# Kernel optimization log

Measured on AMD Instinct MI355X. Metric: run time of the kernel, lower is better.

The kernel has to match this reference:

```python
import jax, jax.numpy as jnp
import numpy as np

N_NODES = 100_000
N_EDGES = 800_000
D = 96
BN_EPS = 1e-5
LEAKY_SLOPE = 0.01


def setup_inputs() -> dict:
    key = jax.random.key(0)
    ks = jax.random.split(key, 9)
    x = jax.random.normal(ks[0], (N_NODES, D), dtype=jnp.float32)
    edge_index = jax.random.randint(ks[1], (2, N_EDGES), 0, N_NODES, dtype=jnp.int64)
    s = 0.05
    return {
        "x": x,
        "edge_index": edge_index,
        # SAGEConv #1 (mean aggregator, bias=False)
        "W_self1": jax.random.normal(ks[2], (D, D), dtype=jnp.float32) * s,
        "W_neigh1": jax.random.normal(ks[3], (D, D), dtype=jnp.float32) * s,
        # SAGEConv #2 (pool aggregator): fc_pool has bias, fc_self/fc_neigh bias=False
        "W_pool": jax.random.normal(ks[4], (D, D), dtype=jnp.float32) * s,
        "b_pool": jax.random.normal(ks[5], (D,), dtype=jnp.float32) * s,
        "W_self2": jax.random.normal(ks[6], (D, D), dtype=jnp.float32) * s,
        "W_neigh2": jax.random.normal(ks[7], (D, D), dtype=jnp.float32) * s,
        # BatchNorm affine params
        "g1": jnp.ones((D,), jnp.float32),
        "beta1": jnp.zeros((D,), jnp.float32),
        "g2": jnp.ones((D,), jnp.float32),
        "beta2": jnp.zeros((D,), jnp.float32),
    }


def _batch_norm(h, gamma, beta):
    # training-mode BatchNorm1d: biased batch stats over nodes
    mu = h.mean(axis=0)
    var = jnp.mean(jnp.square(h - mu), axis=0)
    return gamma * (h - mu) * jax.lax.rsqrt(var + BN_EPS) + beta


def _forward(x, edge_index, W_self1, W_neigh1, W_pool, b_pool, W_self2, W_neigh2,
             g1, beta1, g2, beta2):
    src, dst = edge_index[0], edge_index[1]
    n = x.shape[0]
    deg = jax.ops.segment_sum(jnp.ones((src.shape[0],), x.dtype), dst, num_segments=n)

    # ---- SAGEConv (mean): h_neigh = mean_{u in N(v)} x_u ; out = x W_self + h_neigh W_neigh
    agg_sum = jax.ops.segment_sum(x[src], dst, num_segments=n)          # [N, D]
    h_mean = agg_sum / jnp.maximum(deg, 1.0)[:, None]                   # 0 for isolated nodes
    out1 = x @ W_self1 + h_mean @ W_neigh1
    out1 = _batch_norm(out1, g1, beta1)

    # ---- SAGEConv (pool): h_neigh = max_{u in N(v)} relu(x_u W_pool + b_pool)
    hp = jax.nn.relu(x @ W_pool + b_pool)                               # [N, D]
    agg_max = jax.ops.segment_max(hp[src], dst, num_segments=n)        # -inf where empty
    h_max = jnp.where(deg[:, None] > 0, agg_max, 0.0)
    out2 = x @ W_self2 + h_max @ W_neigh2
    out2 = _batch_norm(out2, g2, beta2)

    return jax.nn.leaky_relu(out1 + out2, negative_slope=LEAKY_SLOPE)


def reference(x, edge_index, W_self1, W_neigh1, W_pool, b_pool, W_self2, W_neigh2,
              g1, beta1, g2, beta2):
    return _forward(x, edge_index, W_self1, W_neigh1, W_pool, b_pool,
                    W_self2, W_neigh2, g1, beta1, g2, beta2)
```

## Files before the change

kernel.cpp:

```cpp
#include <hip/hip_runtime.h>

#define NN 100000
#define NE 800000
#define DD 96
#define NROWPAD 100096
#define GBLK 782
#define SCAN_BLOCKS 100
#define SCAN_CHUNK 1000

typedef __attribute__((ext_vector_type(8))) short bf16x8;
typedef __attribute__((ext_vector_type(8))) unsigned short u16x8;
typedef __attribute__((ext_vector_type(4))) float f32x4;
typedef unsigned short u16;
typedef unsigned int u32;

#define MFMA16 __builtin_amdgcn_mfma_f32_16x16x32_bf16

#define OFF_DEG      0u
#define OFF_ROWSTART 100000u
#define OFF_CURSOR   200004u
#define OFF_BSUM     300004u
#define OFF_STATS    302180u
#define OFF_WT       302948u
#define OFF_CSR      325988u
#define OFF_XH       1125988u
#define OFF_HMBF     10735204u
#define OFF_HXBF     15539812u

__device__ __forceinline__ u16 f2b(float f) {
  u32 u = __float_as_uint(f);
  u += 0x7FFFu + ((u >> 16) & 1u);
  return (u16)(u >> 16);
}
__device__ __forceinline__ float b2f(short h) {
  return __uint_as_float(((u32)(u16)h) << 16);
}

__global__ void wprep_kernel(const float* __restrict__ Ws1, const float* __restrict__ Wn1,
                             const float* __restrict__ Ws2, const float* __restrict__ Wn2,
                             const float* __restrict__ Wp, u16* __restrict__ wt) {
  int idx = blockIdx.x * 256 + threadIdx.x;
  if (idx >= 5 * 9216) return;
  int m = idx / 9216, r = idx % 9216;
  int k = r / 96, c = r % 96;
  const float* W = (m == 0) ? Ws1 : (m == 1) ? Wn1 : (m == 2) ? Ws2 : (m == 3) ? Wn2 : Wp;
  wt[m * 9216 + c * 96 + k] = f2b(W[k * 96 + c]);
}

__global__ void deg_kernel(const int* __restrict__ dst, int* __restrict__ deg) {
  int e = blockIdx.x * blockDim.x + threadIdx.x;
  if (e >= NE) return;
  atomicAdd(&deg[dst[e]], 1);
}

__global__ void scan_sum_kernel(const int* __restrict__ deg, int* __restrict__ bsum) {
  __shared__ int red[256];
  int t = threadIdx.x;
  int base = blockIdx.x * SCAN_CHUNK;
  int s = 0;
  for (int i = t; i < SCAN_CHUNK; i += 256) s += deg[base + i];
  red[t] = s;
  __syncthreads();
  for (int off = 128; off > 0; off >>= 1) {
    if (t < off) red[t] += red[t + off];
    __syncthreads();
  }
  if (t == 0) bsum[blockIdx.x] = red[0];
}

__global__ void scan_bsum_kernel(int* __restrict__ bsum, int* __restrict__ row_start) {
  __shared__ int sm[128];
  int t = threadIdx.x;
  int v = (t < SCAN_BLOCKS) ? bsum[t] : 0;
  sm[t] = v;
  __syncthreads();
  for (int off = 1; off < 128; off <<= 1) {
    int u = 0;
    if (t >= off) u = sm[t - off];
    __syncthreads();
    if (t >= off) sm[t] += u;
    __syncthreads();
  }
  if (t < SCAN_BLOCKS) bsum[t] = sm[t] - v;
  if (t == SCAN_BLOCKS - 1) row_start[NN] = sm[t];
}

__global__ void scan_final_kernel(const int* __restrict__ deg,
                                  const int* __restrict__ bsum,
                                  int* __restrict__ row_start,
                                  int* __restrict__ cursor) {
  __shared__ int sm[256];
  int t = threadIdx.x;
  int base = blockIdx.x * SCAN_CHUNK + t * 4;
  int4 d = {0, 0, 0, 0};
  if (t < 250) d = *reinterpret_cast<const int4*>(deg + base);
  int tot = d.x + d.y + d.z + d.w;
  sm[t] = tot;
  __syncthreads();
  for (int off = 1; off < 256; off <<= 1) {
    int u = 0;
    if (t >= off) u = sm[t - off];
    __syncthreads();
    if (t >= off) sm[t] += u;
    __syncthreads();
  }
  if (t < 250) {
    int run = bsum[blockIdx.x] + sm[t] - tot;
    int4 rs;
    rs.x = run;
    rs.y = run + d.x;
    rs.z = run + d.x + d.y;
    rs.w = run + d.x + d.y + d.z;
    *reinterpret_cast<int4*>(row_start + base) = rs;
    *reinterpret_cast<int4*>(cursor + base) = rs;
  }
}

__global__ void fill_csr_kernel(const int* __restrict__ src,
                                const int* __restrict__ dst,
                                int* __restrict__ cursor,
                                int* __restrict__ csr) {
  int e = blockIdx.x * blockDim.x + threadIdx.x;
  if (e >= NE) return;
  int pos = atomicAdd(&cursor[dst[e]], 1);
  csr[pos] = src[e];
}

__global__ __launch_bounds__(512) void hp_gemm_kernel(const float* __restrict__ x,
                                                      const u16* __restrict__ wt,
                                                      const float* __restrict__ bp,
                                                      u16* __restrict__ xh) {
  __shared__ bf16x8 wl[1152];
  int t = threadIdx.x;
  const bf16x8* wg = reinterpret_cast<const bf16x8*>(wt + 4 * 9216);
  for (int j = t; j < 1152; j += 512) wl[j] = wg[j];
  __syncthreads();
  int w = t >> 6, lane = t & 63;
  int i = lane & 15, g = lane >> 4;
  int row_base = blockIdx.x * 128 + w * 16;
  int grow_a = row_base + i;
  int lrow = grow_a < NN ? grow_a : NN - 1;
  const float4* xr = reinterpret_cast<const float4*>(x + (size_t)lrow * 96);
  bf16x8* xhv = reinterpret_cast<bf16x8*>(xh);
  bf16x8 ax[3];
#pragma unroll
  for (int kb = 0; kb < 3; ++kb) {
    float4 p = xr[(kb * 4 + g) * 2];
    float4 q = xr[(kb * 4 + g) * 2 + 1];
    bf16x8 v;
    v[0] = (short)f2b(p.x); v[1] = (short)f2b(p.y); v[2] = (short)f2b(p.z); v[3] = (short)f2b(p.w);
    v[4] = (short)f2b(q.x); v[5] = (short)f2b(q.y); v[6] = (short)f2b(q.z); v[7] = (short)f2b(q.w);
    ax[kb] = v;
    xhv[(size_t)grow_a * 24 + kb * 4 + g] = v;
  }
  for (int nt = 0; nt < 6; ++nt) {
    f32x4 acc = {0.f, 0.f, 0.f, 0.f};
    int bch = (nt * 16 + i) * 12;
#pragma unroll
    for (int kb = 0; kb < 3; ++kb)
      acc = MFMA16(ax[kb], wl[bch + kb * 4 + g], acc, 0, 0, 0);
    int col = nt * 16 + i;
    float bias = bp[col];
#pragma unroll
    for (int r = 0; r < 4; ++r) {
      int grow = row_base + g * 4 + r;
      xh[(size_t)grow * 192 + 96 + col] = f2b(fmaxf(acc[r] + bias, 0.0f));
    }
  }
}

__global__ __launch_bounds__(256) void gather_kernel(const u16* __restrict__ xh,
                                                     const int* __restrict__ row_start,
                                                     const int* __restrict__ csr,
                                                     u16* __restrict__ hmbf,
                                                     u16* __restrict__ hxbf) {
  int t = threadIdx.x;
  int node = blockIdx.x * 32 + (t & 31);
  int slot = t >> 5;
  bool isMax = slot >= 4;
  if (node >= NN) return;
  int beg = row_start[node], end = row_start[node + 1];
  int last = (end > beg) ? (end - 1) : 0;
  int cbase = slot * 3;
  const u16x8* XH = reinterpret_cast<const u16x8*>(xh);
  float s0[8], s1[8], s2[8];
  u16x8 m0, m1, m2;
#pragma unroll
  for (int j = 0; j < 8; ++j) {
    s0[j] = 0.f; s1[j] = 0.f; s2[j] = 0.f;
    m0[j] = 0; m1[j] = 0; m2[j] = 0;
  }
  int e = beg;
  int i0 = csr[(beg < end) ? beg : 0];
  int i1 = csr[(beg + 1 <= last) ? beg + 1 : last];
  int i2 = csr[(beg + 2 <= last) ? beg + 2 : last];
  int i3 = csr[(beg + 3 <= last) ? beg + 3 : last];
  for (; e + 4 <= end; e += 4) {
    int p = e + 4;
    int n0 = csr[(p     <= last) ? p     : last];
    int n1 = csr[(p + 1 <= last) ? p + 1 : last];
    int n2 = csr[(p + 2 <= last) ? p + 2 : last];
    int n3 = csr[(p + 3 <= last) ? p + 3 : last];
    size_t b0 = (size_t)i0 * 24 + cbase;
    size_t b1 = (size_t)i1 * 24 + cbase;
    size_t b2 = (size_t)i2 * 24 + cbase;
    size_t b3 = (size_t)i3 * 24 + cbase;
    u16x8 a0 = XH[b0], a1 = XH[b0 + 1], a2 = XH[b0 + 2];
    u16x8 c0 = XH[b1], c1 = XH[b1 + 1], c2 = XH[b1 + 2];
    u16x8 d0 = XH[b2], d1 = XH[b2 + 1], d2 = XH[b2 + 2];
    u16x8 f0 = XH[b3], f1 = XH[b3 + 1], f2 = XH[b3 + 2];
    if (isMax) {
#pragma unroll
      for (int j = 0; j < 8; ++j) {
        u16 p0 = a0[j] > c0[j] ? a0[j] : c0[j];
        u16 q0 = d0[j] > f0[j] ? d0[j] : f0[j];
        u16 r0 = p0 > q0 ? p0 : q0;
        m0[j] = m0[j] > r0 ? m0[j] : r0;
        u16 p1 = a1[j] > c1[j] ? a1[j] : c1[j];
        u16 q1 = d1[j] > f1[j] ? d1[j] : f1[j];
        u16 r1 = p1 > q1 ? p1 : q1;
        m1[j] = m1[j] > r1 ? m1[j] : r1;
        u16 p2 = a2[j] > c2[j] ? a2[j] : c2[j];
        u16 q2 = d2[j] > f2[j] ? d2[j] : f2[j];
        u16 r2 = p2 > q2 ? p2 : q2;
        m2[j] = m2[j] > r2 ? m2[j] : r2;
      }
    } else {
#pragma unroll
      for (int j = 0; j < 8; ++j) {
        s0[j] += (b2f((short)a0[j]) + b2f((short)c0[j])) + (b2f((short)d0[j]) + b2f((short)f0[j]));
        s1[j] += (b2f((short)a1[j]) + b2f((short)c1[j])) + (b2f((short)d1[j]) + b2f((short)f1[j]));
        s2[j] += (b2f((short)a2[j]) + b2f((short)c2[j])) + (b2f((short)d2[j]) + b2f((short)f2[j]));
      }
    }
    i0 = n0; i1 = n1; i2 = n2; i3 = n3;
  }
  int rem = end - e;
#pragma unroll
  for (int k = 0; k < 3; ++k) {
    if (k < rem) {
      int ik = (k == 0) ? i0 : (k == 1) ? i1 : i2;
      size_t b0 = (size_t)ik * 24 + cbase;
      u16x8 a0 = XH[b0], a1 = XH[b0 + 1], a2 = XH[b0 + 2];
      if (isMax) {
#pragma unroll
        for (int j = 0; j < 8; ++j) {
          m0[j] = m0[j] > a0[j] ? m0[j] : a0[j];
          m1[j] = m1[j] > a1[j] ? m1[j] : a1[j];
          m2[j] = m2[j] > a2[j] ? m2[j] : a2[j];
        }
      } else {
#pragma unroll
        for (int j = 0; j < 8; ++j) {
          s0[j] += b2f((short)a0[j]);
          s1[j] += b2f((short)a1[j]);
          s2[j] += b2f((short)a2[j]);
        }
      }
    }
  }
  if (isMax) {
    u16x8* dv = reinterpret_cast<u16x8*>(hxbf);
    size_t ob = (size_t)node * 12 + (slot - 4) * 3;
    dv[ob] = m0; dv[ob + 1] = m1; dv[ob + 2] = m2;
  } else {
    float scl = (end > beg) ? 1.0f / (float)(end - beg) : 0.0f;
    u16x8 w0, w1, w2;
#pragma unroll
    for (int j = 0; j < 8; ++j) {
      w0[j] = f2b(s0[j] * scl);
      w1[j] = f2b(s1[j] * scl);
      w2[j] = f2b(s2[j] * scl);
    }
    u16x8* dv = reinterpret_cast<u16x8*>(hmbf);
    size_t ob = (size_t)node * 12 + slot * 3;
    dv[ob] = w0; dv[ob + 1] = w1; dv[ob + 2] = w2;
  }
}

__global__ __launch_bounds__(512, 6) void stats_gemm_kernel(const u16* __restrict__ xh,
                                                            const u16* __restrict__ hmbf,
                                                            const u16* __restrict__ hxbf,
                                                            const u16* __restrict__ wt,
                                                            float* __restrict__ stats) {
  __shared__ bf16x8 wl[2304];
  __shared__ float smst[384];
  int t = threadIdx.x;
  const bf16x8* wg = reinterpret_cast<const bf16x8*>(wt);
  for (int j = t; j < 2304; j += 512) wl[j] = wg[j];
  for (int j = t; j < 384; j += 512) smst[j] = 0.f;
  __syncthreads();
  int w = t >> 6, lane = t & 63;
  int i = lane & 15, g = lane >> 4;
  int row_base = blockIdx.x * 128 + w * 16;
  size_t arowx = (size_t)(row_base + i) * 24;
  size_t arowh = (size_t)(row_base + i) * 12;
  const bf16x8* X = reinterpret_cast<const bf16x8*>(xh);
  const bf16x8* M = reinterpret_cast<const bf16x8*>(hmbf);
  const bf16x8* H = reinterpret_cast<const bf16x8*>(hxbf);
  bf16x8 ax0 = X[arowx + g], ax1 = X[arowx + 4 + g], ax2 = X[arowx + 8 + g];
  {
    bf16x8 am0 = M[arowh + g], am1 = M[arowh + 4 + g], am2 = M[arowh + 8 + g];
#pragma unroll
    for (int nt = 0; nt < 6; ++nt) {
      f32x4 a1 = {0.f, 0.f, 0.f, 0.f};
      int bch = (nt * 16 + i) * 12 + g;
      a1 = MFMA16(ax0, wl[bch], a1, 0, 0, 0);
      a1 = MFMA16(ax1, wl[bch + 4], a1, 0, 0, 0);
      a1 = MFMA16(ax2, wl[bch + 8], a1, 0, 0, 0);
      a1 = MFMA16(am0, wl[1152 + bch], a1, 0, 0, 0);
      a1 = MFMA16(am1, wl[1152 + bch + 4], a1, 0, 0, 0);
      a1 = MFMA16(am2, wl[1152 + bch + 8], a1, 0, 0, 0);
      int col = nt * 16 + i;
      float s1 = 0, q1 = 0;
#pragma unroll
      for (int r = 0; r < 4; ++r) {
        int grow = row_base + g * 4 + r;
        if (grow < NN) { float v = a1[r]; s1 += v; q1 += v * v; }
      }
      s1 += __shfl_xor(s1, 16); q1 += __shfl_xor(q1, 16);
      s1 += __shfl_xor(s1, 32); q1 += __shfl_xor(q1, 32);
      if (g == 0) {
        atomicAdd(&smst[col], s1);
        atomicAdd(&smst[96 + col], q1);
      }
    }
  }
  __syncthreads();
  for (int j = t; j < 2304; j += 512) wl[j] = wg[2304 + j];
  __syncthreads();
  {
    bf16x8 ah0 = H[arowh + g], ah1 = H[arowh + 4 + g], ah2 = H[arowh + 8 + g];
#pragma unroll
    for (int nt = 0; nt < 6; ++nt) {
      f32x4 a2 = {0.f, 0.f, 0.f, 0.f};
      int bch = (nt * 16 + i) * 12 + g;
      a2 = MFMA16(ax0, wl[bch], a2, 0, 0, 0);
      a2 = MFMA16(ax1, wl[bch + 4], a2, 0, 0, 0);
      a2 = MFMA16(ax2, wl[bch + 8], a2, 0, 0, 0);
      a2 = MFMA16(ah0, wl[1152 + bch], a2, 0, 0, 0);
      a2 = MFMA16(ah1, wl[1152 + bch + 4], a2, 0, 0, 0);
      a2 = MFMA16(ah2, wl[1152 + bch + 8], a2, 0, 0, 0);
      int col = nt * 16 + i;
      float s2 = 0, q2 = 0;
#pragma unroll
      for (int r = 0; r < 4; ++r) {
        int grow = row_base + g * 4 + r;
        if (grow < NN) { float v = a2[r]; s2 += v; q2 += v * v; }
      }
      s2 += __shfl_xor(s2, 16); q2 += __shfl_xor(q2, 16);
      s2 += __shfl_xor(s2, 32); q2 += __shfl_xor(q2, 32);
      if (g == 0) {
        atomicAdd(&smst[192 + col], s2);
        atomicAdd(&smst[288 + col], q2);
      }
    }
  }
  __syncthreads();
  for (int j = t; j < 384; j += 512) atomicAdd(&stats[j], smst[j]);
}

__global__ __launch_bounds__(512, 4) void out_gemm_kernel(const u16* __restrict__ xh,
                                                          const u16* __restrict__ hmbf,
                                                          const u16* __restrict__ hxbf,
                                                          const u16* __restrict__ wt,
                                                          const float* __restrict__ stats,
                                                          const float* __restrict__ g1,
                                                          const float* __restrict__ beta1,
                                                          const float* __restrict__ g2,
                                                          const float* __restrict__ beta2,
                                                          float* __restrict__ out) {
  __shared__ bf16x8 wl[2304];
  __shared__ float pl[384];
  int t = threadIdx.x;
  const bf16x8* wg = reinterpret_cast<const bf16x8*>(wt);
  for (int j = t; j < 2304; j += 512) wl[j] = wg[j];
  if (t < 96) {
    const float inv_n = 1.0f / NN;
    float mu1 = stats[t] * inv_n;
    float var1 = fmaxf(stats[96 + t] * inv_n - mu1 * mu1, 0.0f);
    float a1 = g1[t] * rsqrtf(var1 + 1e-5f);
    pl[t] = a1;
    pl[96 + t] = beta1[t] - a1 * mu1;
    float mu2 = stats[192 + t] * inv_n;
    float var2 = fmaxf(stats[288 + t] * inv_n - mu2 * mu2, 0.0f);
    float a2 = g2[t] * rsqrtf(var2 + 1e-5f);
    pl[192 + t] = a2;
    pl[288 + t] = beta2[t] - a2 * mu2;
  }
  __syncthreads();
  int w = t >> 6, lane = t & 63;
  int i = lane & 15, g = lane >> 4;
  int row_base = blockIdx.x * 128 + w * 16;
  size_t arowx = (size_t)(row_base + i) * 24;
  size_t arowh = (size_t)(row_base + i) * 12;
  const bf16x8* X = reinterpret_cast<const bf16x8*>(xh);
  const bf16x8* M = reinterpret_cast<const bf16x8*>(hmbf);
  const bf16x8* H = reinterpret_cast<const bf16x8*>(hxbf);
  bf16x8 ax0 = X[arowx + g], ax1 = X[arowx + 4 + g], ax2 = X[arowx + 8 + g];
  f32x4 o1[6];
  {
    bf16x8 am0 = M[arowh + g], am1 = M[arowh + 4 + g], am2 = M[arowh + 8 + g];
#pragma unroll
    for (int nt = 0; nt < 6; ++nt) {
      f32x4 a1 = {0.f, 0.f, 0.f, 0.f};
      int bch = (nt * 16 + i) * 12 + g;
      a1 = MFMA16(ax0, wl[bch], a1, 0, 0, 0);
      a1 = MFMA16(ax1, wl[bch + 4], a1, 0, 0, 0);
      a1 = MFMA16(ax2, wl[bch + 8], a1, 0, 0, 0);
      a1 = MFMA16(am0, wl[1152 + bch], a1, 0, 0, 0);
      a1 = MFMA16(am1, wl[1152 + bch + 4], a1, 0, 0, 0);
      a1 = MFMA16(am2, wl[1152 + bch + 8], a1, 0, 0, 0);
      o1[nt] = a1;
    }
  }
  __syncthreads();
  for (int j = t; j < 2304; j += 512) wl[j] = wg[2304 + j];
  __syncthreads();
  {
    bf16x8 ah0 = H[arowh + g], ah1 = H[arowh + 4 + g], ah2 = H[arowh + 8 + g];
#pragma unroll
    for (int nt = 0; nt < 6; ++nt) {
      f32x4 a2 = {0.f, 0.f, 0.f, 0.f};
      int bch = (nt * 16 + i) * 12 + g;
      a2 = MFMA16(ax0, wl[bch], a2, 0, 0, 0);
      a2 = MFMA16(ax1, wl[bch + 4], a2, 0, 0, 0);
      a2 = MFMA16(ax2, wl[bch + 8], a2, 0, 0, 0);
      a2 = MFMA16(ah0, wl[1152 + bch], a2, 0, 0, 0);
      a2 = MFMA16(ah1, wl[1152 + bch + 4], a2, 0, 0, 0);
      a2 = MFMA16(ah2, wl[1152 + bch + 8], a2, 0, 0, 0);
      int col = nt * 16 + i;
      float p1 = pl[col], c1 = pl[96 + col];
      float p2 = pl[192 + col], c2 = pl[288 + col];
#pragma unroll
      for (int r = 0; r < 4; ++r) {
        int grow = row_base + g * 4 + r;
        if (grow < NN) {
          float v = p1 * o1[nt][r] + c1 + p2 * a2[r] + c2;
          v = v > 0.f ? v : 0.01f * v;
          out[(size_t)grow * 96 + col] = v;
        }
      }
    }
  }
}

extern "C" void kernel_launch(void* const* d_in, const int* in_sizes, int n_in,
                              void* d_out, int out_size, void* d_ws, size_t ws_size,
                              hipStream_t stream) {
  const float* x       = (const float*)d_in[0];
  const int*   ei      = (const int*)d_in[1];
  const float* W_self1 = (const float*)d_in[2];
  const float* W_neigh1= (const float*)d_in[3];
  const float* W_pool  = (const float*)d_in[4];
  const float* b_pool  = (const float*)d_in[5];
  const float* W_self2 = (const float*)d_in[6];
  const float* W_neigh2= (const float*)d_in[7];
  const float* g1      = (const float*)d_in[8];
  const float* beta1   = (const float*)d_in[9];
  const float* g2      = (const float*)d_in[10];
  const float* beta2   = (const float*)d_in[11];
  float* out = (float*)d_out;

  float* ws = (float*)d_ws;
  int*   deg       = (int*)(ws + OFF_DEG);
  int*   row_start = (int*)(ws + OFF_ROWSTART);
  int*   cursor    = (int*)(ws + OFF_CURSOR);
  int*   bsum      = (int*)(ws + OFF_BSUM);
  float* stats     = ws + OFF_STATS;
  u16*   wt        = (u16*)(ws + OFF_WT);
  int*   csr       = (int*)(ws + OFF_CSR);
  u16*   xh        = (u16*)(ws + OFF_XH);
  u16*   hmbf      = (u16*)(ws + OFF_HMBF);
  u16*   hxbf      = (u16*)(ws + OFF_HXBF);

  const int* src = ei;
  const int* dst = ei + NE;

  hipMemsetAsync(deg, 0, NN * sizeof(int), stream);
  hipMemsetAsync(stats, 0, 384 * sizeof(float), stream);

  wprep_kernel<<<(5 * 9216 + 255) / 256, 256, 0, stream>>>(W_self1, W_neigh1, W_self2,
                                                           W_neigh2, W_pool, wt);

  deg_kernel<<<(NE + 255) / 256, 256, 0, stream>>>(dst, deg);
  scan_sum_kernel<<<SCAN_BLOCKS, 256, 0, stream>>>(deg, bsum);
  scan_bsum_kernel<<<1, 128, 0, stream>>>(bsum, row_start);
  scan_final_kernel<<<SCAN_BLOCKS, 256, 0, stream>>>(deg, bsum, row_start, cursor);
  fill_csr_kernel<<<(NE + 255) / 256, 256, 0, stream>>>(src, dst, cursor, csr);

  hp_gemm_kernel<<<GBLK, 512, 0, stream>>>(x, wt, b_pool, xh);

  gather_kernel<<<(NN + 31) / 32, 256, 0, stream>>>(xh, row_start, csr, hmbf, hxbf);

  stats_gemm_kernel<<<GBLK, 512, 0, stream>>>(xh, hmbf, hxbf, wt, stats);
  out_gemm_kernel<<<GBLK, 512, 0, stream>>>(xh, hmbf, hxbf, wt, stats,
                                            g1, beta1, g2, beta2, out);
}
```

Before: 262.6 us.

## Store bf16 GEMM outputs once and apply BatchNorm in elementwise pass

The stats GEMM now writes its bf16-rounded pre-BatchNorm outputs in place over the aggregation buffers, staging them through shared memory for coalesced stores. A small finalize kernel computes the per-channel scale and shift, and a vectorized elementwise kernel applies BN and leaky ReLU. This replaces the second full GEMM pass that recomputed both products. In exchange the pre-BN activations are rounded to bf16, which costs precision, and there is extra intermediate write and read traffic plus one more launch.

```diff
diff --git a/kernel.cpp b/kernel.cpp
--- a/kernel.cpp
+++ b/kernel.cpp
@@ -21,6 +21,7 @@
 #define OFF_CURSOR   200004u
 #define OFF_BSUM     300004u
 #define OFF_STATS    302180u
+#define OFF_PARAMS   302564u
 #define OFF_WT       302948u
 #define OFF_CSR      325988u
 #define OFF_XH       1125988u
@@ -278,13 +279,14 @@
   }
 }
 
-__global__ __launch_bounds__(512, 6) void stats_gemm_kernel(const u16* __restrict__ xh,
-                                                            const u16* __restrict__ hmbf,
-                                                            const u16* __restrict__ hxbf,
-                                                            const u16* __restrict__ wt,
-                                                            float* __restrict__ stats) {
+__global__ __launch_bounds__(512, 4) void ogemm_kernel(const u16* __restrict__ xh,
+                                                       u16* __restrict__ hmbf,
+                                                       u16* __restrict__ hxbf,
+                                                       const u16* __restrict__ wt,
+                                                       float* __restrict__ stats) {
   __shared__ bf16x8 wl[2304];
   __shared__ float smst[384];
+  __shared__ __align__(16) u16 ot[128][104];
   int t = threadIdx.x;
   const bf16x8* wg = reinterpret_cast<const bf16x8*>(wt);
   for (int j = t; j < 2304; j += 512) wl[j] = wg[j];
@@ -293,6 +295,7 @@
   int w = t >> 6, lane = t & 63;
   int i = lane & 15, g = lane >> 4;
   int row_base = blockIdx.x * 128 + w * 16;
+  int row0 = blockIdx.x * 128;
   size_t arowx = (size_t)(row_base + i) * 24;
   size_t arowh = (size_t)(row_base + i) * 12;
   const bf16x8* X = reinterpret_cast<const bf16x8*>(xh);
@@ -315,8 +318,9 @@
       float s1 = 0, q1 = 0;
 #pragma unroll
       for (int r = 0; r < 4; ++r) {
-        int grow = row_base + g * 4 + r;
-        if (grow < NN) { float v = a1[r]; s1 += v; q1 += v * v; }
+        int lrow = w * 16 + g * 4 + r;
+        ot[lrow][col] = f2b(a1[r]);
+        if (row0 + lrow < NN) { float v = a1[r]; s1 += v; q1 += v * v; }
       }
       s1 += __shfl_xor(s1, 16); q1 += __shfl_xor(q1, 16);
       s1 += __shfl_xor(s1, 32); q1 += __shfl_xor(q1, 32);
@@ -327,7 +331,17 @@
     }
   }
   __syncthreads();
-  for (int j = t; j < 2304; j += 512) wl[j] = wg[2304 + j];
+  {
+    u16x8* dv = reinterpret_cast<u16x8*>(hmbf);
+#pragma unroll
+    for (int c = 0; c < 3; ++c) {
+      int ci = t + c * 512;
+      int r = ci / 12, cc = ci % 12;
+      u16x8 v = *reinterpret_cast<const u16x8*>(&ot[r][cc * 8]);
+      dv[(size_t)(row0 + r) * 12 + cc] = v;
+    }
+    for (int j = t; j < 2304; j += 512) wl[j] = wg[2304 + j];
+  }
   __syncthreads();
   {
     bf16x8 ah0 = H[arowh + g], ah1 = H[arowh + 4 + g], ah2 = H[arowh + 8 + g];
@@ -345,8 +359,9 @@
       float s2 = 0, q2 = 0;
 #pragma unroll
       for (int r = 0; r < 4; ++r) {
-        int grow = row_base + g * 4 + r;
-        if (grow < NN) { float v = a2[r]; s2 += v; q2 += v * v; }
+        int lrow = w * 16 + g * 4 + r;
+        ot[lrow][col] = f2b(a2[r]);
+        if (row0 + lrow < NN) { float v = a2[r]; s2 += v; q2 += v * v; }
       }
       s2 += __shfl_xor(s2, 16); q2 += __shfl_xor(q2, 16);
       s2 += __shfl_xor(s2, 32); q2 += __shfl_xor(q2, 32);
@@ -357,92 +372,68 @@
     }
   }
   __syncthreads();
+  {
+    u16x8* dv = reinterpret_cast<u16x8*>(hxbf);
+#pragma unroll
+    for (int c = 0; c < 3; ++c) {
+      int ci = t + c * 512;
+      int r = ci / 12, cc = ci % 12;
+      u16x8 v = *reinterpret_cast<const u16x8*>(&ot[r][cc * 8]);
+      dv[(size_t)(row0 + r) * 12 + cc] = v;
+    }
+  }
   for (int j = t; j < 384; j += 512) atomicAdd(&stats[j], smst[j]);
 }
 
-__global__ __launch_bounds__(512, 4) void out_gemm_kernel(const u16* __restrict__ xh,
-                                                          const u16* __restrict__ hmbf,
-                                                          const u16* __restrict__ hxbf,
-                                                          const u16* __restrict__ wt,
-                                                          const float* __restrict__ stats,
-                                                          const float* __restrict__ g1,
-                                                          const float* __restrict__ beta1,
-                                                          const float* __restrict__ g2,
-                                                          const float* __restrict__ beta2,
-                                                          float* __restrict__ out) {
-  __shared__ bf16x8 wl[2304];
-  __shared__ float pl[384];
-  int t = threadIdx.x;
-  const bf16x8* wg = reinterpret_cast<const bf16x8*>(wt);
-  for (int j = t; j < 2304; j += 512) wl[j] = wg[j];
-  if (t < 96) {
-    const float inv_n = 1.0f / NN;
-    float mu1 = stats[t] * inv_n;
-    float var1 = fmaxf(stats[96 + t] * inv_n - mu1 * mu1, 0.0f);
-    float a1 = g1[t] * rsqrtf(var1 + 1e-5f);
-    pl[t] = a1;
-    pl[96 + t] = beta1[t] - a1 * mu1;
-    float mu2 = stats[192 + t] * inv_n;
-    float var2 = fmaxf(stats[288 + t] * inv_n - mu2 * mu2, 0.0f);
-    float a2 = g2[t] * rsqrtf(var2 + 1e-5f);
-    pl[192 + t] = a2;
-    pl[288 + t] = beta2[t] - a2 * mu2;
-  }
-  __syncthreads();
-  int w = t >> 6, lane = t & 63;
-  int i = lane & 15, g = lane >> 4;
-  int row_base = blockIdx.x * 128 + w * 16;
-  size_t arowx = (size_t)(row_base + i) * 24;
-  size_t arowh = (size_t)(row_base + i) * 12;
-  const bf16x8* X = reinterpret_cast<const bf16x8*>(xh);
-  const bf16x8* M = reinterpret_cast<const bf16x8*>(hmbf);
-  const bf16x8* H = reinterpret_cast<const bf16x8*>(hxbf);
-  bf16x8 ax0 = X[arowx + g], ax1 = X[arowx + 4 + g], ax2 = X[arowx + 8 + g];
-  f32x4 o1[6];
-  {
-    bf16x8 am0 = M[arowh + g], am1 = M[arowh + 4 + g], am2 = M[arowh + 8 + g];
-#pragma unroll
-    for (int nt = 0; nt < 6; ++nt) {
-      f32x4 a1 = {0.f, 0.f, 0.f, 0.f};
-      int bch = (nt * 16 + i) * 12 + g;
-      a1 = MFMA16(ax0, wl[bch], a1, 0, 0, 0);
-      a1 = MFMA16(ax1, wl[bch + 4], a1, 0, 0, 0);
-      a1 = MFMA16(ax2, wl[bch + 8], a1, 0, 0, 0);
-      a1 = MFMA16(am0, wl[1152 + bch], a1, 0, 0, 0);
-      a1 = MFMA16(am1, wl[1152 + bch + 4], a1, 0, 0, 0);
-      a1 = MFMA16(am2, wl[1152 + bch + 8], a1, 0, 0, 0);
-      o1[nt] = a1;
-    }
-  }
-  __syncthreads();
-  for (int j = t; j < 2304; j += 512) wl[j] = wg[2304 + j];
-  __syncthreads();
-  {
-    bf16x8 ah0 = H[arowh + g], ah1 = H[arowh + 4 + g], ah2 = H[arowh + 8 + g];
-#pragma unroll
-    for (int nt = 0; nt < 6; ++nt) {
-      f32x4 a2 = {0.f, 0.f, 0.f, 0.f};
-      int bch = (nt * 16 + i) * 12 + g;
-      a2 = MFMA16(ax0, wl[bch], a2, 0, 0, 0);
-      a2 = MFMA16(ax1, wl[bch + 4], a2, 0, 0, 0);
-      a2 = MFMA16(ax2, wl[bch + 8], a2, 0, 0, 0);
-      a2 = MFMA16(ah0, wl[1152 + bch], a2, 0, 0, 0);
-      a2 = MFMA16(ah1, wl[1152 + bch + 4], a2, 0, 0, 0);
-      a2 = MFMA16(ah2, wl[1152 + bch + 8], a2, 0, 0, 0);
-      int col = nt * 16 + i;
-      float p1 = pl[col], c1 = pl[96 + col];
-      float p2 = pl[192 + col], c2 = pl[288 + col];
-#pragma unroll
-      for (int r = 0; r < 4; ++r) {
-        int grow = row_base + g * 4 + r;
-        if (grow < NN) {
-          float v = p1 * o1[nt][r] + c1 + p2 * a2[r] + c2;
-          v = v > 0.f ? v : 0.01f * v;
-          out[(size_t)grow * 96 + col] = v;
-        }
-      }
-    }
-  }
+__global__ void finalize_kernel(const float* __restrict__ stats,
+                                const float* __restrict__ g1, const float* __restrict__ beta1,
+                                const float* __restrict__ g2, const float* __restrict__ beta2,
+                                float* __restrict__ params) {
+  int c = threadIdx.x;
+  if (c >= 96) return;
+  const float inv_n = 1.0f / NN;
+  float mu1 = stats[c] * inv_n;
+  float var1 = fmaxf(stats[96 + c] * inv_n - mu1 * mu1, 0.0f);
+  float is1 = rsqrtf(var1 + 1e-5f);
+  float a1 = g1[c] * is1;
+  params[c] = a1;
+  params[96 + c] = beta1[c] - a1 * mu1;
+  float mu2 = stats[192 + c] * inv_n;
+  float var2 = fmaxf(stats[288 + c] * inv_n - mu2 * mu2, 0.0f);
+  float is2 = rsqrtf(var2 + 1e-5f);
+  float a2 = g2[c] * is2;
+  params[192 + c] = a2;
+  params[288 + c] = beta2[c] - a2 * mu2;
+}
+
+__global__ __launch_bounds__(256) void final_kernel(const u16* __restrict__ o1,
+                                                    const u16* __restrict__ o2,
+                                                    const float* __restrict__ params,
+                                                    float* __restrict__ out) {
+  int idx = blockIdx.x * 256 + threadIdx.x;
+  if (idx >= NN * 12) return;
+  int c8 = idx % 12;
+  bf16x8 v1 = reinterpret_cast<const bf16x8*>(o1)[idx];
+  bf16x8 v2 = reinterpret_cast<const bf16x8*>(o2)[idx];
+  const float4* P = reinterpret_cast<const float4*>(params);
+  float4 A1l = P[c8 * 2],      A1h = P[c8 * 2 + 1];
+  float4 B1l = P[24 + c8 * 2], B1h = P[24 + c8 * 2 + 1];
+  float4 A2l = P[48 + c8 * 2], A2h = P[48 + c8 * 2 + 1];
+  float4 B2l = P[72 + c8 * 2], B2h = P[72 + c8 * 2 + 1];
+  float A1[8] = {A1l.x, A1l.y, A1l.z, A1l.w, A1h.x, A1h.y, A1h.z, A1h.w};
+  float B1[8] = {B1l.x, B1l.y, B1l.z, B1l.w, B1h.x, B1h.y, B1h.z, B1h.w};
+  float A2[8] = {A2l.x, A2l.y, A2l.z, A2l.w, A2h.x, A2h.y, A2h.z, A2h.w};
+  float B2[8] = {B2l.x, B2l.y, B2l.z, B2l.w, B2h.x, B2h.y, B2h.z, B2h.w};
+  float o[8];
+#pragma unroll
+  for (int j = 0; j < 8; ++j) {
+    float v = A1[j] * b2f((short)v1[j]) + B1[j] + A2[j] * b2f((short)v2[j]) + B2[j];
+    o[j] = v > 0.f ? v : 0.01f * v;
+  }
+  float4* ov = reinterpret_cast<float4*>(out);
+  float4 lo = {o[0], o[1], o[2], o[3]}, hi = {o[4], o[5], o[6], o[7]};
+  ov[idx * 2] = lo;
+  ov[idx * 2 + 1] = hi;
 }
 
 extern "C" void kernel_launch(void* const* d_in, const int* in_sizes, int n_in,
@@ -468,6 +459,7 @@
   int*   cursor    = (int*)(ws + OFF_CURSOR);
   int*   bsum      = (int*)(ws + OFF_BSUM);
   float* stats     = ws + OFF_STATS;
+  float* params    = ws + OFF_PARAMS;
   u16*   wt        = (u16*)(ws + OFF_WT);
   int*   csr       = (int*)(ws + OFF_CSR);
   u16*   xh        = (u16*)(ws + OFF_XH);
@@ -493,7 +485,7 @@
 
   gather_kernel<<<(NN + 31) / 32, 256, 0, stream>>>(xh, row_start, csr, hmbf, hxbf);
 
-  stats_gemm_kernel<<<GBLK, 512, 0, stream>>>(xh, hmbf, hxbf, wt, stats);
-  out_gemm_kernel<<<GBLK, 512, 0, stream>>>(xh, hmbf, hxbf, wt, stats,
-                                            g1, beta1, g2, beta2, out);
-}
+  ogemm_kernel<<<GBLK, 512, 0, stream>>>(xh, hmbf, hxbf, wt, stats);
+  finalize_kernel<<<1, 128, 0, stream>>>(stats, g1, beta1, g2, beta2, params);
+  final_kernel<<<(NN * 12 + 255) / 256, 256, 0, stream>>>(hmbf, hxbf, params, out);
+}
```

Measured after the change: 259.2 us. Within noise of the previous version (-1.3%).
